# Kernel tuning notes

Measured on AMD Instinct MI355X. Metric: run time of the kernel, lower is better.

The kernel has to match this reference:

```python
import jax, jax.numpy as jnp
import numpy as np

Z_DIM = 64
HIDDEN = 400
DATASET = 1000000
EPS = 0.01
S_STEPS = 20
T_STEPS = 5
LOG_2PI = float(np.log(2.0 * np.pi))


def setup_inputs() -> dict:
    key = jax.random.key(0)
    ks = jax.random.split(key, 10)
    B = 16384
    x = jax.random.uniform(ks[0], (B, 1, 28, 28), dtype=jnp.float32)
    indices = jax.random.randint(ks[1], (B,), 0, DATASET, dtype=jnp.int64)
    # MLP params (torch Linear convention: y = x @ W.T + b)
    W1 = jax.random.normal(ks[2], (HIDDEN, 784), dtype=jnp.float32) * 0.03
    b1 = jnp.zeros((HIDDEN,), dtype=jnp.float32)
    W21 = jax.random.normal(ks[3], (Z_DIM, HIDDEN), dtype=jnp.float32) * 0.05
    b21 = jnp.zeros((Z_DIM,), dtype=jnp.float32)
    W22 = jax.random.normal(ks[4], (Z_DIM, HIDDEN), dtype=jnp.float32) * 0.05
    b22 = jnp.zeros((Z_DIM,), dtype=jnp.float32)
    cached_samples = jax.random.normal(ks[5], (DATASET, Z_DIM), dtype=jnp.float32)
    # pre-drawn Langevin noise for all s+t steps
    noise = jax.random.normal(ks[6], (S_STEPS + T_STEPS, B, Z_DIM), dtype=jnp.float32)
    return {"x": x, "indices": indices, "K": 1, "W1": W1, "b1": b1,
            "W21": W21, "b21": b21, "W22": W22, "b22": b22,
            "cached_samples": cached_samples, "noise": noise}


def _encode(x, W1, b1, W21, b21, W22, b22):
    xf = x.reshape(-1, 784)
    h = jax.nn.relu(xf @ W1.T + b1)
    z_loc = h @ W21.T + b21
    z_scale = jnp.exp(h @ W22.T + b22)
    return z_loc, z_scale


def _langevin(z0, noise_steps, z_loc, z_scale):
    # ULA: z <- z + eps * grad_log_q(z) + sqrt(2*eps) * xi
    inv_var = 1.0 / (z_scale * z_scale)
    coef = jnp.sqrt(2.0 * EPS).astype(z0.dtype)

    def step(z, xi):
        grad = (z_loc - z) * inv_var
        return z + EPS * grad + coef * xi, None

    z, _ = jax.lax.scan(step, z0, noise_steps)
    return z


def reference(x, indices, K, W1, b1, W21, b21, W22, b22, cached_samples, noise):
    z_loc, z_scale = _encode(x, W1, b1, W21, b21, W22, b22)
    # gather cached particles
    z = cached_samples[indices]
    # s detached steps, then t graph-carrying steps (same math in fwd)
    z = jax.lax.stop_gradient(_langevin(z, noise[:S_STEPS], z_loc, z_scale))
    z = _langevin(z, noise[S_STEPS:], z_loc, z_scale)
    # scatter updated particles back
    new_cache = cached_samples.at[indices].set(jax.lax.stop_gradient(z))
    # Normal log-prob summed over latent dim
    log_qz_x = jnp.sum(
        -0.5 * jnp.square((z - z_loc) / z_scale) - jnp.log(z_scale) - 0.5 * LOG_2PI,
        axis=-1)
    return log_qz_x, z, new_cache
```

## Files before the change

### kernel.cpp

```cpp
#include <hip/hip_runtime.h>


#define ZD 64
#define NSTEPS 25
#define EPSI 0.01f
#define K1 784
#define K1P 800
#define HSTR 512

typedef __attribute__((ext_vector_type(8))) short short8;
typedef __attribute__((ext_vector_type(4))) float f32x4;

__device__ __forceinline__ unsigned short f2bf(float f) {
  union { float f; unsigned u; } v; v.f = f;
  return (unsigned short)((v.u + 0x7FFFu + ((v.u >> 16) & 1u)) >> 16);
}

__device__ __forceinline__ void gload_lds16(const void* g, void* l) {
  __builtin_amdgcn_global_load_lds(
      (const __attribute__((address_space(1))) void*)g,
      (__attribute__((address_space(3))) void*)l, 16, 0, 0);
}

__global__ __launch_bounds__(256) void prep_kernel(
    const float* __restrict__ W1, const float* __restrict__ W21,
    const float* __restrict__ W22, short* __restrict__ W1b,
    short* __restrict__ Wout) {
  const int t = blockIdx.x * 256 + threadIdx.x;
  const int NW1 = 512 * (K1P / 8);
  if (t < NW1) {
    const int n = t / (K1P / 8), k0 = (t % (K1P / 8)) * 8;
    short8 v = {0, 0, 0, 0, 0, 0, 0, 0};
    if (n < 400 && k0 < K1) {
      const float* s = W1 + (long)n * K1 + k0;
#pragma unroll
      for (int e = 0; e < 8; e++) v[e] = (short)f2bf(s[e]);
    }
    *(short8*)(W1b + (long)t * 8) = v;
  } else {
    const int q = t - NW1;
    if (q < 128 * 64) {
      const int n = q / 64, k0 = (q % 64) * 8;
      short8 v = {0, 0, 0, 0, 0, 0, 0, 0};
      if (k0 < 400) {
        const float* s = (n < 64) ? (W21 + (long)n * 400 + k0)
                                  : (W22 + (long)(n - 64) * 400 + k0);
#pragma unroll
        for (int e = 0; e < 8; e++) v[e] = (short)f2bf(s[e]);
      }
      *(short8*)(Wout + (long)q * 8) = v;
    }
  }
}

__global__ __launch_bounds__(512) void gemm1_kernel(
    const float* __restrict__ X, const short* __restrict__ W1b,
    const float* __restrict__ b1, unsigned short* __restrict__ H) {
  __shared__ short As[4 * 64 * 8];
  __shared__ short Bs[32 * 64 * 8];
  const int tid = threadIdx.x;
  const int w = tid >> 6;
  const int lane = tid & 63;
  const int wr = w >> 2;
  const int wc = w & 3;
  const int m0 = blockIdx.x * 64;

  const f32x4 vzero = {0.f, 0.f, 0.f, 0.f};
  f32x4 acc[2][8];
#pragma unroll
  for (int i = 0; i < 2; i++)
#pragma unroll
    for (int j = 0; j < 8; j++) acc[i][j] = vzero;

  for (int k0 = 0; k0 < K1P; k0 += 32) {
    if (k0) __syncthreads();
    if (tid < 256) {
      const int row = m0 + (tid >> 6) * 16 + (lane & 15);
      const int gk = k0 + (lane >> 4) * 8;
      short8 av = {0, 0, 0, 0, 0, 0, 0, 0};
      if (gk < K1) {
        const float4 f0 = *(const float4*)(X + (long)row * K1 + gk);
        const float4 f1 = *(const float4*)(X + (long)row * K1 + gk + 4);
        av[0] = (short)f2bf(f0.x); av[1] = (short)f2bf(f0.y);
        av[2] = (short)f2bf(f0.z); av[3] = (short)f2bf(f0.w);
        av[4] = (short)f2bf(f1.x); av[5] = (short)f2bf(f1.y);
        av[6] = (short)f2bf(f1.z); av[7] = (short)f2bf(f1.w);
      }
      *(short8*)(As + (long)tid * 8) = av;
    }
#pragma unroll
    for (int t = 0; t < 4; t++) {
      const int gn = w * 4 + t;
      const short* src = W1b + (long)(gn * 16 + (lane & 15)) * K1P +
                         k0 + (lane >> 4) * 8;
      gload_lds16(src, Bs + gn * 512);
    }
    __syncthreads();
    const short8* Ap = (const short8*)As;
    const short8* Bp = (const short8*)Bs;
    const short8 a0 = Ap[(wr * 2 + 0) * 64 + lane];
    const short8 a1 = Ap[(wr * 2 + 1) * 64 + lane];
#pragma unroll
    for (int j = 0; j < 8; j++) {
      const short8 b = Bp[(wc * 8 + j) * 64 + lane];
      acc[0][j] = __builtin_amdgcn_mfma_f32_16x16x32_bf16(a0, b, acc[0][j], 0, 0, 0);
      acc[1][j] = __builtin_amdgcn_mfma_f32_16x16x32_bf16(a1, b, acc[1][j], 0, 0, 0);
    }
  }
  const int colg = lane & 15;
  const int rowg = (lane >> 4) * 4;
#pragma unroll
  for (int j = 0; j < 8; j++) {
    const int col = wc * 128 + j * 16 + colg;
    const float bias = (col < 400) ? b1[col] : 0.f;
#pragma unroll
    for (int i = 0; i < 2; i++) {
      const int rbase = m0 + wr * 32 + i * 16 + rowg;
#pragma unroll
      for (int r = 0; r < 4; r++) {
        H[(long)(rbase + r) * HSTR + col] = f2bf(fmaxf(acc[i][j][r] + bias, 0.f));
      }
    }
  }
}

__global__ __launch_bounds__(256) void gemm2_kernel(
    const unsigned short* __restrict__ H, const short* __restrict__ Wout,
    const float* __restrict__ b21, const float* __restrict__ b22,
    float* __restrict__ zloc, float* __restrict__ uarr) {
  __shared__ short As[4 * 64 * 8];
  __shared__ short Bs[8 * 64 * 8];
  const int tid = threadIdx.x;
  const int w = tid >> 6;
  const int lane = tid & 63;
  const int wr = w >> 1;
  const int wc = w & 1;
  const int m0 = blockIdx.x * 64;

  const f32x4 vzero = {0.f, 0.f, 0.f, 0.f};
  f32x4 acc[2][4];
#pragma unroll
  for (int i = 0; i < 2; i++)
#pragma unroll
    for (int j = 0; j < 4; j++) acc[i][j] = vzero;

  for (int k0 = 0; k0 < HSTR; k0 += 32) {
    if (k0) __syncthreads();
    {
      const unsigned short* src = H + (long)(m0 + w * 16 + (lane & 15)) * HSTR +
                                  k0 + (lane >> 4) * 8;
      gload_lds16(src, As + w * 512);
    }
#pragma unroll
    for (int t = 0; t < 2; t++) {
      const int gn = w * 2 + t;
      const short* src = Wout + (long)(gn * 16 + (lane & 15)) * HSTR +
                         k0 + (lane >> 4) * 8;
      gload_lds16(src, Bs + gn * 512);
    }
    __syncthreads();
    const short8* Ap = (const short8*)As;
    const short8* Bp = (const short8*)Bs;
    const short8 a0 = Ap[(wr * 2 + 0) * 64 + lane];
    const short8 a1 = Ap[(wr * 2 + 1) * 64 + lane];
#pragma unroll
    for (int j = 0; j < 4; j++) {
      const short8 b = Bp[(wc * 4 + j) * 64 + lane];
      acc[0][j] = __builtin_amdgcn_mfma_f32_16x16x32_bf16(a0, b, acc[0][j], 0, 0, 0);
      acc[1][j] = __builtin_amdgcn_mfma_f32_16x16x32_bf16(a1, b, acc[1][j], 0, 0, 0);
    }
  }
  const int colg = lane & 15;
  const int rowg = (lane >> 4) * 4;
  float* outp = wc ? uarr : zloc;
  const float* bp = wc ? b22 : b21;
#pragma unroll
  for (int j = 0; j < 4; j++) {
    const int col = j * 16 + colg;
    const float bias = bp[col];
#pragma unroll
    for (int i = 0; i < 2; i++) {
      const int rbase = m0 + wr * 32 + i * 16 + rowg;
#pragma unroll
      for (int r = 0; r < 4; r++) {
        outp[(long)(rbase + r) * ZD + col] = acc[i][j][r] + bias;
      }
    }
  }
}

__global__ void winner_kernel(const int* __restrict__ idx, int* __restrict__ winner, int B) {
  const int j = blockIdx.x * 256 + threadIdx.x;
  if (j < B) atomicMax(&winner[idx[j]], j + 1);
}

__global__ __launch_bounds__(256) void langevin_kernel(
    const float* __restrict__ zloc, const float* __restrict__ uarr,
    const float* __restrict__ cache, const int* __restrict__ idx,
    const float* __restrict__ noise, float* __restrict__ out_logq,
    float* __restrict__ out_z, int B) {
  const int row = blockIdx.x * 4 + (threadIdx.x >> 6);
  const int lane = threadIdx.x & 63;
  const int i = idx[row];
  const float zl = zloc[(long)row * ZD + lane];
  const float uu = uarr[(long)row * ZD + lane];
  const float a = EPSI * expf(-2.f * uu);
  float z = cache[(long)i * ZD + lane];
  const float coef = sqrtf(2.f * EPSI);
  const float* np = noise + (long)row * ZD + lane;
  const long stride = (long)B * ZD;
#pragma unroll
  for (int s = 0; s < NSTEPS; s++) {
    z = z + a * (zl - z) + coef * np[(long)s * stride];
  }
  out_z[(long)row * ZD + lane] = z;
  const float d = (z - zl) * expf(-uu);
  float t = -0.5f * d * d - uu - 0.91893853320467274178f;
#pragma unroll
  for (int off = 1; off < 64; off <<= 1) t += __shfl_xor(t, off);
  if (lane == 0) out_logq[row] = t;
}

__global__ __launch_bounds__(256) void copy_kernel(
    const float4* __restrict__ cache4, const float4* __restrict__ z4,
    const int* __restrict__ winner, float4* __restrict__ out4) {
  const long e = (long)blockIdx.x * 256 + threadIdx.x;
  const long row = e >> 4;
  const int c = (int)(e & 15);
  const int w = winner[row];
  float4 v;
  if (w == 0) v = cache4[e];
  else        v = z4[(long)(w - 1) * 16 + c];
  out4[e] = v;
}

extern "C" void kernel_launch(void* const* d_in, const int* in_sizes, int n_in,
                              void* d_out, int out_size, void* d_ws, size_t ws_size,
                              hipStream_t stream) {
  const float* x     = (const float*)d_in[0];
  const int*   idx   = (const int*)d_in[1];
  const float* W1    = (const float*)d_in[3];
  const float* b1    = (const float*)d_in[4];
  const float* W21   = (const float*)d_in[5];
  const float* b21   = (const float*)d_in[6];
  const float* W22   = (const float*)d_in[7];
  const float* b22   = (const float*)d_in[8];
  const float* cache = (const float*)d_in[9];
  const float* noise = (const float*)d_in[10];

  const int B  = in_sizes[1];
  const int DS = in_sizes[9] / ZD;

  float* out_logq  = (float*)d_out;
  float* out_z     = out_logq + B;
  float* out_cache = out_z + (long)B * ZD;

  unsigned short* h = (unsigned short*)d_ws;
  short* w1b  = (short*)(h + (long)B * HSTR);
  short* wout = w1b + 512 * K1P;
  float* zloc = (float*)(wout + 128 * HSTR);
  float* u    = zloc + (long)B * ZD;
  int*   win  = (int*)(u + (long)B * ZD);

  hipMemsetAsync(win, 0, (size_t)DS * sizeof(int), stream);

  const int prep_chunks = 512 * (K1P / 8) + 128 * 64;
  prep_kernel<<<(prep_chunks + 255) / 256, 256, 0, stream>>>(W1, W21, W22, w1b, wout);
  gemm1_kernel<<<B / 64, 512, 0, stream>>>(x, w1b, b1, h);
  gemm2_kernel<<<B / 64, 256, 0, stream>>>(h, wout, b21, b22, zloc, u);
  winner_kernel<<<(B + 255) / 256, 256, 0, stream>>>(idx, win, B);
  langevin_kernel<<<B / 4, 256, 0, stream>>>(zloc, u, cache, idx, noise,
                                             out_logq, out_z, B);
  const long total4 = (long)DS * (ZD / 4);
  copy_kernel<<<(unsigned)(total4 / 256), 256, 0, stream>>>(
      (const float4*)cache, (const float4*)out_z, win, (float4*)out_cache);
}
```

Measured before the change: 189.4 us.

## Bulk-copy cache and scatter winning particles in Langevin kernel

The per-element winner lookup in the cache copy is dropped. The cache is now copied with a plain nontemporal vector copy, and the Langevin kernel writes each updated particle into the output cache only when its row is the last writer for that index. The full-dataset memset of the winner array is replaced by a kernel that zeroes only the entries named by the indices. This removes the 4 MB winner memset and the per-row winner reads from the dominant copy pass, but it requires the Langevin kernel to run after the copy and adds a grid-stride loop to it.

Measured after the change: 201.9 us. 1.07x slower.

```diff
diff --git a/kernel.cpp b/kernel.cpp
--- a/kernel.cpp
+++ b/kernel.cpp
@@ -51,6 +51,18 @@
       *(short8*)(Wout + (long)q * 8) = v;
     }
   }
+}
+
+__global__ __launch_bounds__(256) void zero_touched_kernel(
+    const int* __restrict__ idx, int* __restrict__ winner, int B) {
+  const int j = blockIdx.x * 256 + threadIdx.x;
+  if (j < B) winner[idx[j]] = 0;
+}
+
+__global__ __launch_bounds__(256) void winner_kernel(
+    const int* __restrict__ idx, int* __restrict__ winner, int B) {
+  const int j = blockIdx.x * 256 + threadIdx.x;
+  if (j < B) atomicMax(&winner[idx[j]], j + 1);
 }
 
 __global__ __launch_bounds__(512) void gemm1_kernel(
@@ -189,49 +201,52 @@
   }
 }
 
-__global__ void winner_kernel(const int* __restrict__ idx, int* __restrict__ winner, int B) {
-  const int j = blockIdx.x * 256 + threadIdx.x;
-  if (j < B) atomicMax(&winner[idx[j]], j + 1);
+#define COPY_BLOCKS 2048
+__global__ __launch_bounds__(256) void copy_kernel(
+    const f32x4* __restrict__ src, f32x4* __restrict__ dst, long n4) {
+  const long base = (long)blockIdx.x * 256 * 32 + threadIdx.x;
+#pragma unroll
+  for (int k = 0; k < 32; k++) {
+    const long e = base + (long)k * 256;
+    if (e < n4) {
+      f32x4 v = __builtin_nontemporal_load(&src[e]);
+      __builtin_nontemporal_store(v, &dst[e]);
+    }
+  }
 }
 
 __global__ __launch_bounds__(256) void langevin_kernel(
     const float* __restrict__ zloc, const float* __restrict__ uarr,
     const float* __restrict__ cache, const int* __restrict__ idx,
-    const float* __restrict__ noise, float* __restrict__ out_logq,
-    float* __restrict__ out_z, int B) {
-  const int row = blockIdx.x * 4 + (threadIdx.x >> 6);
+    const float* __restrict__ noise, const int* __restrict__ winner,
+    float* __restrict__ out_logq, float* __restrict__ out_z,
+    float* __restrict__ out_cache, int B) {
   const int lane = threadIdx.x & 63;
-  const int i = idx[row];
-  const float zl = zloc[(long)row * ZD + lane];
-  const float uu = uarr[(long)row * ZD + lane];
-  const float a = EPSI * expf(-2.f * uu);
-  float z = cache[(long)i * ZD + lane];
+  const int slot = blockIdx.x * 4 + (threadIdx.x >> 6);
+  const int nslots = gridDim.x * 4;
   const float coef = sqrtf(2.f * EPSI);
-  const float* np = noise + (long)row * ZD + lane;
   const long stride = (long)B * ZD;
-#pragma unroll
-  for (int s = 0; s < NSTEPS; s++) {
-    z = z + a * (zl - z) + coef * np[(long)s * stride];
-  }
-  out_z[(long)row * ZD + lane] = z;
-  const float d = (z - zl) * expf(-uu);
-  float t = -0.5f * d * d - uu - 0.91893853320467274178f;
-#pragma unroll
-  for (int off = 1; off < 64; off <<= 1) t += __shfl_xor(t, off);
-  if (lane == 0) out_logq[row] = t;
-}
-
-__global__ __launch_bounds__(256) void copy_kernel(
-    const float4* __restrict__ cache4, const float4* __restrict__ z4,
-    const int* __restrict__ winner, float4* __restrict__ out4) {
-  const long e = (long)blockIdx.x * 256 + threadIdx.x;
-  const long row = e >> 4;
-  const int c = (int)(e & 15);
-  const int w = winner[row];
-  float4 v;
-  if (w == 0) v = cache4[e];
-  else        v = z4[(long)(w - 1) * 16 + c];
-  out4[e] = v;
+  for (int row = slot; row < B; row += nslots) {
+    const int i = idx[row];
+    const float zl = zloc[(long)row * ZD + lane];
+    const float uu = uarr[(long)row * ZD + lane];
+    const float a = EPSI * expf(-2.f * uu);
+    float z = cache[(long)i * ZD + lane];
+    const float* np = noise + (long)row * ZD + lane;
+#pragma unroll
+    for (int s = 0; s < NSTEPS; s++) {
+      z = z + a * (zl - z) + coef * np[(long)s * stride];
+    }
+    out_z[(long)row * ZD + lane] = z;
+    if (winner[i] == row + 1) {
+      out_cache[(long)i * ZD + lane] = z;
+    }
+    const float d = (z - zl) * expf(-uu);
+    float t = -0.5f * d * d - uu - 0.91893853320467274178f;
+#pragma unroll
+    for (int off = 1; off < 64; off <<= 1) t += __shfl_xor(t, off);
+    if (lane == 0) out_logq[row] = t;
+  }
 }
 
 extern "C" void kernel_launch(void* const* d_in, const int* in_sizes, int n_in,
@@ -262,16 +277,18 @@
   float* u    = zloc + (long)B * ZD;
   int*   win  = (int*)(u + (long)B * ZD);
 
-  hipMemsetAsync(win, 0, (size_t)DS * sizeof(int), stream);
+  zero_touched_kernel<<<(B + 255) / 256, 256, 0, stream>>>(idx, win, B);
 
   const int prep_chunks = 512 * (K1P / 8) + 128 * 64;
   prep_kernel<<<(prep_chunks + 255) / 256, 256, 0, stream>>>(W1, W21, W22, w1b, wout);
   gemm1_kernel<<<B / 64, 512, 0, stream>>>(x, w1b, b1, h);
   gemm2_kernel<<<B / 64, 256, 0, stream>>>(h, wout, b21, b22, zloc, u);
   winner_kernel<<<(B + 255) / 256, 256, 0, stream>>>(idx, win, B);
-  langevin_kernel<<<B / 4, 256, 0, stream>>>(zloc, u, cache, idx, noise,
-                                             out_logq, out_z, B);
+
   const long total4 = (long)DS * (ZD / 4);
-  copy_kernel<<<(unsigned)(total4 / 256), 256, 0, stream>>>(
-      (const float4*)cache, (const float4*)out_z, win, (float4*)out_cache);
-}
+  copy_kernel<<<COPY_BLOCKS, 256, 0, stream>>>(
+      (const f32x4*)cache, (f32x4*)out_cache, total4);
+
+  langevin_kernel<<<2048, 256, 0, stream>>>(zloc, u, cache, idx, noise, win,
+                                            out_logq, out_z, out_cache, B);
+}
```
